# Kernel tuning notes

Hardware: AMD Instinct MI355X
Metric: run time of the kernel (lower is better)

## Reference

```python
import jax, jax.numpy as jnp
import numpy as np

ENCODER_DIM = 512
HIDDEN_DIM = 512
ATTENTION_DIM = 512
BATCH = 512
NUM_PIXELS = 196


def setup_inputs() -> dict:
    key = jax.random.key(0)
    ks = jax.random.split(key, 8)
    s_enc = 1.0 / np.sqrt(ENCODER_DIM)
    s_dec = 1.0 / np.sqrt(HIDDEN_DIM)
    s_att = 1.0 / np.sqrt(ATTENTION_DIM)
    return {
        "encoder_out": jax.random.normal(ks[0], (BATCH, NUM_PIXELS, ENCODER_DIM), jnp.float32),
        "decoder_hidden": jax.random.normal(ks[1], (BATCH, HIDDEN_DIM), jnp.float32),
        # enc_att: Linear(encoder_dim -> attention_dim)
        "W_enc": jax.random.uniform(ks[2], (ENCODER_DIM, ATTENTION_DIM), jnp.float32, -s_enc, s_enc),
        "b_enc": jax.random.uniform(ks[3], (ATTENTION_DIM,), jnp.float32, -s_enc, s_enc),
        # dec_att: Linear(hidden_dim -> attention_dim)
        "W_dec": jax.random.uniform(ks[4], (HIDDEN_DIM, ATTENTION_DIM), jnp.float32, -s_dec, s_dec),
        "b_dec": jax.random.uniform(ks[5], (ATTENTION_DIM,), jnp.float32, -s_dec, s_dec),
        # full_att: Linear(attention_dim -> 1)
        "w_full": jax.random.uniform(ks[6], (ATTENTION_DIM,), jnp.float32, -s_att, s_att),
        "b_full": jax.random.uniform(ks[7], (1,), jnp.float32, -s_att, s_att),
    }


def reference(encoder_out, decoder_hidden, W_enc, b_enc, W_dec, b_dec, w_full, b_full):
    # att_enc: [B, P, A]
    att_enc = jnp.einsum('bpe,ea->bpa', encoder_out, W_enc) + b_enc
    # att_dec: [B, 1, A]
    att_dec = (decoder_hidden @ W_dec + b_dec)[:, None, :]
    # energy: [B, P]
    energy = jnp.einsum('bpa,a->bp', jax.nn.relu(att_enc + att_dec), w_full) + b_full[0]
    alpha = jax.nn.softmax(energy, axis=1)  # [B, P]
    context = jnp.einsum('bpe,bp->be', encoder_out, alpha)  # [B, E]
    return context, alpha
```

## Files before the change

### kernel.cpp

```cpp
#include <hip/hip_runtime.h>
#include <hip/hip_bf16.h>
#include <cstdint>

#define KDIM 512
#define BM 128
#define BN 128
#define BK 64
#define M_MAIN 100352
#define NPIX 196
#define BATCH 512

typedef float f32x4 __attribute__((ext_vector_type(4)));
typedef short s16x8 __attribute__((ext_vector_type(8)));
typedef short s16x4 __attribute__((ext_vector_type(4)));

__device__ __forceinline__ short f2bf(float f) {
    uint32_t u = __float_as_uint(f);
    uint32_t r = u + 0x7FFFu + ((u >> 16) & 1u);
    return (short)(r >> 16);
}

__device__ __forceinline__ void gload_lds16(const void* g, void* l) {
    __builtin_amdgcn_global_load_lds(
        (const __attribute__((address_space(1))) void*)g,
        (__attribute__((address_space(3))) void*)l, 16, 0, 0);
}

__global__ void prep_w(const float* __restrict__ W_enc, const float* __restrict__ W_dec,
                       short* __restrict__ Wt_enc, short* __restrict__ Wt_dec) {
    int a = blockIdx.x;
    int k = threadIdx.x;
    const float* W = blockIdx.y ? W_dec : W_enc;
    short* Wt = blockIdx.y ? Wt_dec : Wt_enc;
    Wt[a * KDIM + k] = f2bf(W[(size_t)k * KDIM + a]);
}

template <int EPI>
__launch_bounds__(256, 2)
__global__ void gemm_fused(const float* __restrict__ A, int M,
                           const short* __restrict__ Bt,
                           const float* __restrict__ b1, const float* __restrict__ b2,
                           const float* __restrict__ attdec, const float* __restrict__ wfull,
                           float* __restrict__ outp) {
    __shared__ short lds_a[2][BM][BK];
    __shared__ short lds_b[2][BN][BK];

    const int tid = threadIdx.x;
    const int wave = tid >> 6;
    const int lane = tid & 63;
    const int wm = wave >> 1;
    const int wn = wave & 1;
    const int nwg = gridDim.x;
    const int q = nwg >> 3;
    const int swzb = (blockIdx.x & 7) * q + (blockIdx.x >> 3);
    const int bx = swzb & 3;
    const int by = swzb >> 2;
    const int r0 = by * BM;
    const int c0 = bx * BN;

    f32x4 areg[8];

    auto loadA = [&](int kt) {
#pragma unroll
        for (int j = 0; j < 8; ++j) {
            int f = tid + 256 * j;
            int row = f >> 4, c4 = f & 15;
            areg[j] = *(const f32x4*)(A + (size_t)(r0 + row) * KDIM + kt * BK + c4 * 4);
        }
    };
    auto writeA = [&](int buf) {
#pragma unroll
        for (int j = 0; j < 8; ++j) {
            int f = tid + 256 * j;
            int row = f >> 4;
            int cs = (f & 15) * 4;
            int cw = cs ^ ((row & 7) * 8);
            f32x4 v = areg[j];
            s16x4 o;
            o[0] = f2bf(v[0]); o[1] = f2bf(v[1]); o[2] = f2bf(v[2]); o[3] = f2bf(v[3]);
            *(s16x4*)&lds_a[buf][row][cw] = o;
        }
    };
    auto stageB = [&](int buf, int kt) {
#pragma unroll
        for (int i = 0; i < 4; ++i) {
            int rb = wave * 32 + i * 8;
            int srcslot = (lane & 7) ^ (lane >> 3);
            const short* g = Bt + (size_t)(c0 + rb + (lane >> 3)) * KDIM + kt * BK + srcslot * 8;
            gload_lds16(g, &lds_b[buf][rb][0]);
        }
    };

    f32x4 acc[4][4];
#pragma unroll
    for (int i = 0; i < 4; ++i)
#pragma unroll
        for (int j = 0; j < 4; ++j)
            acc[i][j] = (f32x4){0.f, 0.f, 0.f, 0.f};

    auto compute = [&](int buf) {
#pragma unroll
        for (int kk = 0; kk < 2; ++kk) {
            s16x8 af[4], bf[4];
#pragma unroll
            for (int fm = 0; fm < 4; ++fm) {
                int ra = wm * 64 + fm * 16 + (lane & 15);
                af[fm] = *(const s16x8*)&lds_a[buf][ra][(kk * 32 + (lane >> 4) * 8) ^ ((ra & 7) * 8)];
            }
#pragma unroll
            for (int fn = 0; fn < 4; ++fn) {
                int rb = wn * 64 + fn * 16 + (lane & 15);
                bf[fn] = *(const s16x8*)&lds_b[buf][rb][(kk * 32 + (lane >> 4) * 8) ^ ((rb & 7) * 8)];
            }
#pragma unroll
            for (int fm = 0; fm < 4; ++fm)
#pragma unroll
                for (int fn = 0; fn < 4; ++fn)
                    acc[fm][fn] = __builtin_amdgcn_mfma_f32_16x16x32_bf16(af[fm], bf[fn], acc[fm][fn], 0, 0, 0);
        }
    };

    loadA(0);
    stageB(0, 0);
    writeA(0);
    __syncthreads();

    const int nk = KDIM / BK;
    for (int t = 0; t < nk; ++t) {
        int cur = t & 1;
        if (t + 1 < nk) {
            loadA(t + 1);
            stageB(cur ^ 1, t + 1);
        }
        compute(cur);
        if (t + 1 < nk) writeA(cur ^ 1);
        __syncthreads();
    }

    const int lcol = lane & 15;
    const int lrg = (lane >> 4) * 4;

    if constexpr (EPI == 0) {
#pragma unroll
        for (int fm = 0; fm < 4; ++fm)
#pragma unroll
            for (int fn = 0; fn < 4; ++fn) {
                int col = c0 + wn * 64 + fn * 16 + lcol;
                float bias = b1[col] + b2[col];
#pragma unroll
                for (int reg = 0; reg < 4; ++reg) {
                    int row = r0 + wm * 64 + fm * 16 + lrg + reg;
                    outp[(size_t)row * KDIM + col] = acc[fm][fn][reg] + bias;
                }
            }
    } else {
        float wfv[4];
        int colv[4];
#pragma unroll
        for (int fn = 0; fn < 4; ++fn) {
            colv[fn] = c0 + wn * 64 + fn * 16 + lcol;
            wfv[fn] = wfull[colv[fn]];
        }
        const int slice = bx * 2 + wn;
#pragma unroll
        for (int fm = 0; fm < 4; ++fm) {
#pragma unroll
            for (int reg = 0; reg < 4; ++reg) {
                int row = r0 + wm * 64 + fm * 16 + lrg + reg;
                int b = row / NPIX;
                float es = 0.f;
#pragma unroll
                for (int fn = 0; fn < 4; ++fn) {
                    float v = acc[fm][fn][reg] + attdec[(size_t)b * KDIM + colv[fn]];
                    v = fmaxf(v, 0.f);
                    es = fmaf(v, wfv[fn], es);
                }
#pragma unroll
                for (int m = 1; m < 16; m <<= 1) es += __shfl_xor(es, m);
                if (lcol == 0) outp[(size_t)slice * M + row] = es;
            }
        }
    }
}

__global__ void softmax_ctx(const float* __restrict__ enc, const float* __restrict__ energy8,
                            float* __restrict__ out) {
    const int b = blockIdx.x;
    const int t = threadIdx.x;
    __shared__ float sal[NPIX];
    __shared__ float wred[4];

    float e = -1e30f;
    if (t < NPIX) {
        float s = 0.f;
#pragma unroll
        for (int i = 0; i < 8; ++i) s += energy8[(size_t)i * M_MAIN + b * NPIX + t];
        e = s;
    }
    float m = e;
#pragma unroll
    for (int d = 1; d < 64; d <<= 1) m = fmaxf(m, __shfl_xor(m, d));
    if ((t & 63) == 0) wred[t >> 6] = m;
    __syncthreads();
    m = fmaxf(fmaxf(wred[0], wred[1]), fmaxf(wred[2], wred[3]));

    float ex = (t < NPIX) ? __expf(e - m) : 0.f;
    float sm = ex;
#pragma unroll
    for (int d = 1; d < 64; d <<= 1) sm += __shfl_xor(sm, d);
    __syncthreads();
    if ((t & 63) == 0) wred[t >> 6] = sm;
    __syncthreads();
    sm = wred[0] + wred[1] + wred[2] + wred[3];

    float al = ex / sm;
    if (t < NPIX) {
        sal[t] = al;
        out[BATCH * KDIM + b * NPIX + t] = al;
    }
    __syncthreads();

    float c0 = 0.f, c1 = 0.f;
    const float* eb = enc + (size_t)b * NPIX * KDIM;
    const int col = 2 * t;
    for (int p = 0; p < NPIX; ++p) {
        float a = sal[p];
        float2 v = *(const float2*)(eb + (size_t)p * KDIM + col);
        c0 = fmaf(v.x, a, c0);
        c1 = fmaf(v.y, a, c1);
    }
    out[b * KDIM + col] = c0;
    out[b * KDIM + col + 1] = c1;
}

extern "C" void kernel_launch(void* const* d_in, const int* in_sizes, int n_in,
                              void* d_out, int out_size, void* d_ws, size_t ws_size,
                              hipStream_t stream) {
    const float* encoder = (const float*)d_in[0];
    const float* dec_h   = (const float*)d_in[1];
    const float* W_enc   = (const float*)d_in[2];
    const float* b_enc   = (const float*)d_in[3];
    const float* W_dec   = (const float*)d_in[4];
    const float* b_dec   = (const float*)d_in[5];
    const float* w_full  = (const float*)d_in[6];
    float* out = (float*)d_out;

    short* wt_enc = (short*)d_ws;
    short* wt_dec = wt_enc + 512 * 512;
    float* attdec = (float*)(wt_dec + 512 * 512);
    float* energy8 = attdec + 512 * 512;

    prep_w<<<dim3(512, 2), 512, 0, stream>>>(W_enc, W_dec, wt_enc, wt_dec);

    gemm_fused<0><<<dim3(16), 256, 0, stream>>>(dec_h, 512, wt_dec,
                                                b_enc, b_dec, nullptr, nullptr, attdec);

    gemm_fused<1><<<dim3(4 * (M_MAIN / BM)), 256, 0, stream>>>(encoder, M_MAIN, wt_enc,
                                                               nullptr, nullptr, attdec, w_full, energy8);

    softmax_ctx<<<dim3(BATCH), 256, 0, stream>>>(encoder, energy8, out);
}
```

Before: 181.7 us.

## Widen GEMM tile to 256 columns with 8 waves and reduce energy partials in LDS

Doubles the N tile to 256 and uses 512-thread blocks (8 waves, 2x4), so each encoder row tile is read by 2 blocks instead of 4, roughly halving redundant fp32 reads of the large encoder tensor. The per-wave energy partials are now summed in shared memory, so only 2 energy slices are written instead of 8, which shrinks the softmax input reads. The A staging path moves to 8-wide loads with packed bf16 conversion and 16-byte LDS stores. Occupancy falls to one 512-thread block per CU, and the LDS footprint of the B buffer doubles.

```diff
diff --git a/kernel.cpp b/kernel.cpp
--- a/kernel.cpp
+++ b/kernel.cpp
@@ -4,7 +4,7 @@
 
 #define KDIM 512
 #define BM 128
-#define BN 128
+#define BN 256
 #define BK 64
 #define M_MAIN 100352
 #define NPIX 196
@@ -12,7 +12,6 @@
 
 typedef float f32x4 __attribute__((ext_vector_type(4)));
 typedef short s16x8 __attribute__((ext_vector_type(8)));
-typedef short s16x4 __attribute__((ext_vector_type(4)));
 
 __device__ __forceinline__ short f2bf(float f) {
     uint32_t u = __float_as_uint(f);
@@ -24,6 +23,11 @@
     __builtin_amdgcn_global_load_lds(
         (const __attribute__((address_space(1))) void*)g,
         (__attribute__((address_space(3))) void*)l, 16, 0, 0);
+}
+
+__device__ __forceinline__ uint32_t pkbf(float lo, float hi) {
+    __hip_bfloat162 p = __float22bfloat162_rn(float2{lo, hi});
+    return *reinterpret_cast<uint32_t*>(&p);
 }
 
 __global__ void prep_w(const float* __restrict__ W_enc, const float* __restrict__ W_dec,
@@ -36,7 +40,7 @@
 }
 
 template <int EPI>
-__launch_bounds__(256, 2)
+__launch_bounds__(512, 1)
 __global__ void gemm_fused(const float* __restrict__ A, int M,
                            const short* __restrict__ Bt,
                            const float* __restrict__ b1, const float* __restrict__ b2,
@@ -48,37 +52,40 @@
     const int tid = threadIdx.x;
     const int wave = tid >> 6;
     const int lane = tid & 63;
-    const int wm = wave >> 1;
-    const int wn = wave & 1;
+    const int wm = wave >> 2;
+    const int wn = wave & 3;
     const int nwg = gridDim.x;
     const int q = nwg >> 3;
     const int swzb = (blockIdx.x & 7) * q + (blockIdx.x >> 3);
-    const int bx = swzb & 3;
-    const int by = swzb >> 2;
+    const int bx = swzb & 1;
+    const int by = swzb >> 1;
     const int r0 = by * BM;
     const int c0 = bx * BN;
 
-    f32x4 areg[8];
+    f32x4 areg[2][2];
 
     auto loadA = [&](int kt) {
 #pragma unroll
-        for (int j = 0; j < 8; ++j) {
-            int f = tid + 256 * j;
-            int row = f >> 4, c4 = f & 15;
-            areg[j] = *(const f32x4*)(A + (size_t)(r0 + row) * KDIM + kt * BK + c4 * 4);
+        for (int c = 0; c < 2; ++c) {
+            int g = tid + 512 * c;
+            int row = g >> 3, col8 = (g & 7) * 8;
+            const float* p = A + (size_t)(r0 + row) * KDIM + kt * BK + col8;
+            areg[c][0] = *(const f32x4*)p;
+            areg[c][1] = *(const f32x4*)(p + 4);
         }
     };
     auto writeA = [&](int buf) {
 #pragma unroll
-        for (int j = 0; j < 8; ++j) {
-            int f = tid + 256 * j;
-            int row = f >> 4;
-            int cs = (f & 15) * 4;
-            int cw = cs ^ ((row & 7) * 8);
-            f32x4 v = areg[j];
-            s16x4 o;
-            o[0] = f2bf(v[0]); o[1] = f2bf(v[1]); o[2] = f2bf(v[2]); o[3] = f2bf(v[3]);
-            *(s16x4*)&lds_a[buf][row][cw] = o;
+        for (int c = 0; c < 2; ++c) {
+            int g = tid + 512 * c;
+            int row = g >> 3;
+            int slot = (g & 7) ^ (row & 7);
+            uint4 w;
+            w.x = pkbf(areg[c][0][0], areg[c][0][1]);
+            w.y = pkbf(areg[c][0][2], areg[c][0][3]);
+            w.z = pkbf(areg[c][1][0], areg[c][1][1]);
+            w.w = pkbf(areg[c][1][2], areg[c][1][3]);
+            *reinterpret_cast<uint4*>(&lds_a[buf][row][slot * 8]) = w;
         }
     };
     auto stageB = [&](int buf, int kt) {
@@ -105,12 +112,14 @@
 #pragma unroll
             for (int fm = 0; fm < 4; ++fm) {
                 int ra = wm * 64 + fm * 16 + (lane & 15);
-                af[fm] = *(const s16x8*)&lds_a[buf][ra][(kk * 32 + (lane >> 4) * 8) ^ ((ra & 7) * 8)];
+                int sl = (kk * 4 + (lane >> 4)) ^ (ra & 7);
+                af[fm] = *(const s16x8*)&lds_a[buf][ra][sl * 8];
             }
 #pragma unroll
             for (int fn = 0; fn < 4; ++fn) {
                 int rb = wn * 64 + fn * 16 + (lane & 15);
-                bf[fn] = *(const s16x8*)&lds_b[buf][rb][(kk * 32 + (lane >> 4) * 8) ^ ((rb & 7) * 8)];
+                int sl = (kk * 4 + (lane >> 4)) ^ (rb & 7);
+                bf[fn] = *(const s16x8*)&lds_b[buf][rb][sl * 8];
             }
 #pragma unroll
             for (int fm = 0; fm < 4; ++fm)
@@ -161,7 +170,7 @@
             colv[fn] = c0 + wn * 64 + fn * 16 + lcol;
             wfv[fn] = wfull[colv[fn]];
         }
-        const int slice = bx * 2 + wn;
+        float* ebuf = reinterpret_cast<float*>(lds_a);
 #pragma unroll
         for (int fm = 0; fm < 4; ++fm) {
 #pragma unroll
@@ -177,13 +186,18 @@
                 }
 #pragma unroll
                 for (int m = 1; m < 16; m <<= 1) es += __shfl_xor(es, m);
-                if (lcol == 0) outp[(size_t)slice * M + row] = es;
-            }
-        }
-    }
-}
-
-__global__ void softmax_ctx(const float* __restrict__ enc, const float* __restrict__ energy8,
+                if (lcol == 0) ebuf[wn * BM + wm * 64 + fm * 16 + lrg + reg] = es;
+            }
+        }
+        __syncthreads();
+        if (tid < BM) {
+            float s = (ebuf[tid] + ebuf[BM + tid]) + (ebuf[2 * BM + tid] + ebuf[3 * BM + tid]);
+            outp[(size_t)bx * M + r0 + tid] = s;
+        }
+    }
+}
+
+__global__ void softmax_ctx(const float* __restrict__ enc, const float* __restrict__ energy2,
                             float* __restrict__ out) {
     const int b = blockIdx.x;
     const int t = threadIdx.x;
@@ -192,9 +206,7 @@
 
     float e = -1e30f;
     if (t < NPIX) {
-        float s = 0.f;
-#pragma unroll
-        for (int i = 0; i < 8; ++i) s += energy8[(size_t)i * M_MAIN + b * NPIX + t];
+        float s = energy2[b * NPIX + t] + energy2[(size_t)M_MAIN + b * NPIX + t];
         e = s;
     }
     float m = e;
@@ -240,23 +252,23 @@
     const float* dec_h   = (const float*)d_in[1];
     const float* W_enc   = (const float*)d_in[2];
     const float* b_enc   = (const float*)d_in[3];
+    const float* b_decv  = (const float*)d_in[5];
     const float* W_dec   = (const float*)d_in[4];
-    const float* b_dec   = (const float*)d_in[5];
     const float* w_full  = (const float*)d_in[6];
     float* out = (float*)d_out;
 
     short* wt_enc = (short*)d_ws;
     short* wt_dec = wt_enc + 512 * 512;
     float* attdec = (float*)(wt_dec + 512 * 512);
-    float* energy8 = attdec + 512 * 512;
+    float* energy2 = attdec + 512 * 512;
 
     prep_w<<<dim3(512, 2), 512, 0, stream>>>(W_enc, W_dec, wt_enc, wt_dec);
 
-    gemm_fused<0><<<dim3(16), 256, 0, stream>>>(dec_h, 512, wt_dec,
-                                                b_enc, b_dec, nullptr, nullptr, attdec);
-
-    gemm_fused<1><<<dim3(4 * (M_MAIN / BM)), 256, 0, stream>>>(encoder, M_MAIN, wt_enc,
-                                                               nullptr, nullptr, attdec, w_full, energy8);
-
-    softmax_ctx<<<dim3(BATCH), 256, 0, stream>>>(encoder, energy8, out);
-}
+    gemm_fused<0><<<dim3(8), 512, 0, stream>>>(dec_h, 512, wt_dec,
+                                               b_enc, b_decv, nullptr, nullptr, attdec);
+
+    gemm_fused<1><<<dim3(2 * (M_MAIN / BM)), 512, 0, stream>>>(encoder, M_MAIN, wt_enc,
+                                                               nullptr, nullptr, attdec, w_full, energy2);
+
+    softmax_ctx<<<dim3(BATCH), 256, 0, stream>>>(encoder, energy2, out);
+}
```

New measurement: 164.8 us. -9.3%, faster.
